# Kernel tuning notes

Measured on AMD Instinct MI355X. Metric: run time of the kernel, lower is better.

Reference implementation:

```python
import jax, jax.numpy as jnp
import numpy as np

B, R, T = 32, 256, 4096  # shots, receivers, time samples; P = T prob grid
EPS = 1e-8


def _trapz(y, t):
    # trapezoidal integral along last axis
    dt = t[1:] - t[:-1]
    return jnp.sum(0.5 * (y[..., 1:] + y[..., :-1]) * dt, axis=-1)


def _cum_trap(y, t):
    # cumulative trapezoid along last axis, prepend 0 -> same length as y
    dt = t[1:] - t[:-1]
    incr = 0.5 * (y[..., 1:] + y[..., :-1]) * dt
    c = jnp.cumsum(incr, axis=-1)
    return jnp.concatenate([jnp.zeros_like(c[..., :1]), c], axis=-1)


def _renorm(x, t):
    # square + trapz-normalize each trace to a probability density over t
    pdf = x * x + EPS
    return pdf / _trapz(pdf, t)[..., None]


def setup_inputs() -> dict:
    key = jax.random.key(0)
    k1, k2 = jax.random.split(key)
    traces = 0.5 * jax.random.normal(k1, (B, R, T), dtype=jnp.float32)
    t = jnp.arange(T, dtype=jnp.float32) * 1e-3
    p = jnp.linspace(0.0, 1.0, T, dtype=jnp.float32)  # probability grid
    # q_raw = true_quantile(obs_data, t, p): invert the observed CDF per trace
    obs = 0.5 * jax.random.normal(k2, (B, R, T), dtype=jnp.float32)
    obs_pdf = _renorm(obs, t)
    obs_cdf = _cum_trap(obs_pdf, t)  # strictly increasing (pdf > 0)
    q_raw = jax.vmap(lambda c: jnp.interp(p, c, t))(obs_cdf.reshape(-1, T))
    q_raw = q_raw.reshape(B, R, T).astype(jnp.float32)
    return {"traces": traces, "t": t, "p": p, "q_raw": q_raw}


def reference(traces, t, p, q_raw):
    pdf = _renorm(traces, t)          # [B,R,T]
    cdf = _cum_trap(pdf, t)           # [B,R,T], in [0,1]
    # quantile lookup: interpolate each trace's quantile table at its cdf values
    cdf_f = cdf.reshape(-1, T)
    q_f = q_raw.reshape(-1, T)
    transport = jax.vmap(jnp.interp, in_axes=(0, None, 0))(cdf_f, p, q_f)
    transport = transport.reshape(pdf.shape)
    diff = t - transport
    loss = jnp.sum(_trapz(diff * diff * pdf, t))
    return loss
```

## Files before the change

### kernel.cpp

```cpp
#include <hip/hip_runtime.h>

#define TT 4096
#define BLK 256
#define PER 16
#define TPB 8
#define EPSV 1e-8f

__device__ __forceinline__ void async_q16(const float* __restrict__ g, float* l) {
  __builtin_amdgcn_global_load_lds(
      (const __attribute__((address_space(1))) void*)g,
      (__attribute__((address_space(3))) void*)l,
      16, 0, 0);
}

__global__ __launch_bounds__(BLK, 4) void w2_loss_kernel(
    const float* __restrict__ traces,
    const float* __restrict__ q_raw,
    float* __restrict__ part) {
  __shared__ float qb[2][TT];
  __shared__ float wave_sums[4];
  __shared__ float wave_red[4];

  const int tid = threadIdx.x;
  const int wv = tid >> 6;
  const int lane = tid & 63;
  const long trace0 = (long)blockIdx.x * TPB;
  const int base = tid * PER;

  {
    const float* qr = q_raw + trace0 * (long)TT;
#pragma unroll
    for (int j = 0; j < 4; ++j) {
      const int c = (wv * 4 + j) * 256;
      async_q16(qr + c + lane * 4, &qb[0][c]);
    }
  }
  float4 trv[4];
  float nb;
  {
    const float* tr = traces + trace0 * (long)TT;
    const float4* tr4 = (const float4*)(tr + base);
#pragma unroll
    for (int j = 0; j < 4; ++j) trv[j] = tr4[j];
    nb = (base + PER < TT) ? tr[base + PER] : 0.0f;
  }

  for (int k = 0; k < TPB; ++k) {
    const int buf = k & 1;
    const long trace = trace0 + k;

    float s[PER + 1];
#pragma unroll
    for (int j = 0; j < 4; ++j) {
      s[4 * j + 0] = trv[j].x * trv[j].x + EPSV;
      s[4 * j + 1] = trv[j].y * trv[j].y + EPSV;
      s[4 * j + 2] = trv[j].z * trv[j].z + EPSV;
      s[4 * j + 3] = trv[j].w * trv[j].w + EPSV;
    }
    s[PER] = (base + PER < TT) ? (nb * nb + EPSV) : 0.0f;

    float lc[PER + 1];
    lc[0] = 0.0f;
#pragma unroll
    for (int m = 0; m < PER; ++m) {
      float t0 = (float)(base + m) * 1e-3f;
      float t1 = (float)(base + m + 1) * 1e-3f;
      float incr = (base + m < TT - 1) ? 0.5f * (s[m] + s[m + 1]) * (t1 - t0)
                                       : 0.0f;
      lc[m + 1] = lc[m] + incr;
    }
    const float tot = lc[PER];

    float v = tot;
#pragma unroll
    for (int off = 1; off < 64; off <<= 1) {
      float n = __shfl_up(v, off, 64);
      if (lane >= off) v += n;
    }
    if (lane == 63) wave_sums[wv] = v;
    __syncthreads();

    if (k + 1 < TPB) {
      const float* qr_n = q_raw + (trace + 1) * (long)TT;
#pragma unroll
      for (int j = 0; j < 4; ++j) {
        const int c = (wv * 4 + j) * 256;
        async_q16(qr_n + c + lane * 4, &qb[buf ^ 1][c]);
      }
      const float* tr_n = traces + (trace + 1) * (long)TT;
      const float4* tr4_n = (const float4*)(tr_n + base);
#pragma unroll
      for (int j = 0; j < 4; ++j) trv[j] = tr4_n[j];
      nb = (base + PER < TT) ? tr_n[base + PER] : 0.0f;
    }

    float wave_off = 0.0f;
    if (wv > 0) wave_off += wave_sums[0];
    if (wv > 1) wave_off += wave_sums[1];
    if (wv > 2) wave_off += wave_sums[2];
    const float excl = (v - tot) + wave_off;
    const float norm = wave_sums[0] + wave_sums[1] + wave_sums[2] + wave_sums[3];
    const float inv_norm = 1.0f / norm;

    const float* __restrict__ lq = qb[buf];
    float local = 0.0f;
#pragma unroll
    for (int m = 0; m < PER; ++m) {
      float x = (excl + lc[m]) * inv_norm;
      float u = x * (float)(TT - 1);
      int i0 = (int)floorf(u);
      i0 = (i0 < 0) ? 0 : ((i0 > TT - 2) ? TT - 2 : i0);
      float f = u - (float)i0;
      f = fminf(fmaxf(f, 0.0f), 1.0f);
      float q0 = lq[i0];
      float q1 = lq[i0 + 1];
      float transport = q0 + f * (q1 - q0);
      float tm = (float)(base + m) * 1e-3f;
      float d = tm - transport;
      float tlo = (float)((base + m == 0) ? 0 : (base + m - 1)) * 1e-3f;
      float thi = (float)((base + m == TT - 1) ? (TT - 1) : (base + m + 1)) * 1e-3f;
      float w = 0.5f * (thi - tlo);
      local += d * d * s[m] * w;
    }
    local *= inv_norm;

#pragma unroll
    for (int off = 32; off > 0; off >>= 1) local += __shfl_down(local, off, 64);
    if (lane == 0) wave_red[wv] = local;
    __syncthreads();
    if (tid == 0) {
      part[trace] = wave_red[0] + wave_red[1] + wave_red[2] + wave_red[3];
    }
  }
}

__global__ __launch_bounds__(BLK) void reduce_kernel(
    const float* __restrict__ part, float* __restrict__ out, int n) {
  __shared__ float wave_red[4];
  const int tid = threadIdx.x;
  float local = 0.0f;
  for (int i = tid; i < n; i += BLK) local += part[i];
#pragma unroll
  for (int off = 32; off > 0; off >>= 1) local += __shfl_down(local, off, 64);
  if ((tid & 63) == 0) wave_red[tid >> 6] = local;
  __syncthreads();
  if (tid == 0) out[0] = wave_red[0] + wave_red[1] + wave_red[2] + wave_red[3];
}

extern "C" void kernel_launch(void* const* d_in, const int* in_sizes, int n_in,
                              void* d_out, int out_size, void* d_ws, size_t ws_size,
                              hipStream_t stream) {
  const float* traces = (const float*)d_in[0];
  const float* q_raw  = (const float*)d_in[3];
  float* out = (float*)d_out;
  float* part = (float*)d_ws;

  const int n_traces = in_sizes[0] / TT;
  const int n_blocks = n_traces / TPB;
  w2_loss_kernel<<<n_blocks, BLK, 0, stream>>>(traces, q_raw, part);
  reduce_kernel<<<1, BLK, 0, stream>>>(part, out, n_traces);
}
```

Measured before the change: 295.7 us.

## Cut LDS and registers to raise occupancy, single-buffer quantile table

Halves traces per block and drops the double-buffered quantile table to one LDS buffer. The launch bound now asks for twice as many resident blocks. The per-element partial CDF array is no longer stored; it is recomputed on the fly in the interpolation loop, and the squared values are kept in place in the float4 registers. Trace loads stay double-buffered, but the next quantile table is only fetched after the block's final barrier. The aim is latency hiding through occupancy instead of in-block overlap, at the cost of less prefetch overlap for the q table and some redundant arithmetic.

```diff
diff --git a/kernel.cpp b/kernel.cpp
--- a/kernel.cpp
+++ b/kernel.cpp
@@ -3,21 +3,29 @@
 #define TT 4096
 #define BLK 256
 #define PER 16
-#define TPB 8
+#define TPB 4
 #define EPSV 1e-8f
 
-__device__ __forceinline__ void async_q16(const float* __restrict__ g, float* l) {
+__device__ __forceinline__ void async_q16(const float* g, float* l) {
   __builtin_amdgcn_global_load_lds(
       (const __attribute__((address_space(1))) void*)g,
-      (__attribute__((address_space(3))) void*)l,
-      16, 0, 0);
+      (__attribute__((address_space(3))) void*)l, 16, 0, 0);
 }
 
-__global__ __launch_bounds__(BLK, 4) void w2_loss_kernel(
+__device__ __forceinline__ float fcomp(const float4& v, int c) {
+  switch (c) {
+    case 0: return v.x;
+    case 1: return v.y;
+    case 2: return v.z;
+    default: return v.w;
+  }
+}
+
+__global__ __launch_bounds__(BLK, 8) void w2_loss_kernel(
     const float* __restrict__ traces,
     const float* __restrict__ q_raw,
     float* __restrict__ part) {
-  __shared__ float qb[2][TT];
+  __shared__ float qb[TT];
   __shared__ float wave_sums[4];
   __shared__ float wave_red[4];
 
@@ -27,49 +35,50 @@
   const long trace0 = (long)blockIdx.x * TPB;
   const int base = tid * PER;
 
+  float4 trv[2][4];
+  float nbuf[2];
   {
+    const float* tr = traces + trace0 * (long)TT;
+    const float4* tr4 = (const float4*)(tr + base);
+#pragma unroll
+    for (int j = 0; j < 4; ++j) trv[0][j] = tr4[j];
+    nbuf[0] = (tid < BLK - 1) ? tr[base + PER] : 0.0f;
     const float* qr = q_raw + trace0 * (long)TT;
 #pragma unroll
     for (int j = 0; j < 4; ++j) {
       const int c = (wv * 4 + j) * 256;
-      async_q16(qr + c + lane * 4, &qb[0][c]);
+      async_q16(qr + c + lane * 4, &qb[c]);
     }
   }
-  float4 trv[4];
-  float nb;
-  {
-    const float* tr = traces + trace0 * (long)TT;
-    const float4* tr4 = (const float4*)(tr + base);
+
 #pragma unroll
-    for (int j = 0; j < 4; ++j) trv[j] = tr4[j];
-    nb = (base + PER < TT) ? tr[base + PER] : 0.0f;
-  }
-
   for (int k = 0; k < TPB; ++k) {
-    const int buf = k & 1;
+    const int cur = k & 1, nxt = cur ^ 1;
     const long trace = trace0 + k;
 
-    float s[PER + 1];
 #pragma unroll
     for (int j = 0; j < 4; ++j) {
-      s[4 * j + 0] = trv[j].x * trv[j].x + EPSV;
-      s[4 * j + 1] = trv[j].y * trv[j].y + EPSV;
-      s[4 * j + 2] = trv[j].z * trv[j].z + EPSV;
-      s[4 * j + 3] = trv[j].w * trv[j].w + EPSV;
+      trv[cur][j].x = trv[cur][j].x * trv[cur][j].x + EPSV;
+      trv[cur][j].y = trv[cur][j].y * trv[cur][j].y + EPSV;
+      trv[cur][j].z = trv[cur][j].z * trv[cur][j].z + EPSV;
+      trv[cur][j].w = trv[cur][j].w * trv[cur][j].w + EPSV;
     }
-    s[PER] = (base + PER < TT) ? (nb * nb + EPSV) : 0.0f;
+    const float s16 = (tid < BLK - 1) ? (nbuf[cur] * nbuf[cur] + EPSV) : 0.0f;
 
-    float lc[PER + 1];
-    lc[0] = 0.0f;
+    float tot = 0.0f;
+    {
+      float t0 = (float)base * 1e-3f;
 #pragma unroll
-    for (int m = 0; m < PER; ++m) {
-      float t0 = (float)(base + m) * 1e-3f;
-      float t1 = (float)(base + m + 1) * 1e-3f;
-      float incr = (base + m < TT - 1) ? 0.5f * (s[m] + s[m + 1]) * (t1 - t0)
-                                       : 0.0f;
-      lc[m + 1] = lc[m] + incr;
+      for (int m = 0; m < PER; ++m) {
+        float t1 = (float)(base + m + 1) * 1e-3f;
+        float sm = fcomp(trv[cur][m >> 2], m & 3);
+        float sm1 = (m < PER - 1) ? fcomp(trv[cur][(m + 1) >> 2], (m + 1) & 3) : s16;
+        float incr = 0.5f * (sm + sm1) * (t1 - t0);
+        if (m == PER - 1) incr = (tid < BLK - 1) ? incr : 0.0f;
+        tot = tot + incr;
+        t0 = t1;
+      }
     }
-    const float tot = lc[PER];
 
     float v = tot;
 #pragma unroll
@@ -80,20 +89,6 @@
     if (lane == 63) wave_sums[wv] = v;
     __syncthreads();
 
-    if (k + 1 < TPB) {
-      const float* qr_n = q_raw + (trace + 1) * (long)TT;
-#pragma unroll
-      for (int j = 0; j < 4; ++j) {
-        const int c = (wv * 4 + j) * 256;
-        async_q16(qr_n + c + lane * 4, &qb[buf ^ 1][c]);
-      }
-      const float* tr_n = traces + (trace + 1) * (long)TT;
-      const float4* tr4_n = (const float4*)(tr_n + base);
-#pragma unroll
-      for (int j = 0; j < 4; ++j) trv[j] = tr4_n[j];
-      nb = (base + PER < TT) ? tr_n[base + PER] : 0.0f;
-    }
-
     float wave_off = 0.0f;
     if (wv > 0) wave_off += wave_sums[0];
     if (wv > 1) wave_off += wave_sums[1];
@@ -102,25 +97,44 @@
     const float norm = wave_sums[0] + wave_sums[1] + wave_sums[2] + wave_sums[3];
     const float inv_norm = 1.0f / norm;
 
-    const float* __restrict__ lq = qb[buf];
+    if (k + 1 < TPB) {
+      const float* trn = traces + (trace + 1) * (long)TT;
+      const float4* tr4n = (const float4*)(trn + base);
+#pragma unroll
+      for (int j = 0; j < 4; ++j) trv[nxt][j] = tr4n[j];
+      nbuf[nxt] = (tid < BLK - 1) ? trn[base + PER] : 0.0f;
+    }
+
     float local = 0.0f;
+    {
+      float tlo = (tid == 0) ? 0.0f : (float)(base - 1) * 1e-3f;
+      float tm = (float)base * 1e-3f;
+      float lcm = 0.0f;
 #pragma unroll
-    for (int m = 0; m < PER; ++m) {
-      float x = (excl + lc[m]) * inv_norm;
-      float u = x * (float)(TT - 1);
-      int i0 = (int)floorf(u);
-      i0 = (i0 < 0) ? 0 : ((i0 > TT - 2) ? TT - 2 : i0);
-      float f = u - (float)i0;
-      f = fminf(fmaxf(f, 0.0f), 1.0f);
-      float q0 = lq[i0];
-      float q1 = lq[i0 + 1];
-      float transport = q0 + f * (q1 - q0);
-      float tm = (float)(base + m) * 1e-3f;
-      float d = tm - transport;
-      float tlo = (float)((base + m == 0) ? 0 : (base + m - 1)) * 1e-3f;
-      float thi = (float)((base + m == TT - 1) ? (TT - 1) : (base + m + 1)) * 1e-3f;
-      float w = 0.5f * (thi - tlo);
-      local += d * d * s[m] * w;
+      for (int m = 0; m < PER; ++m) {
+        float thi = (float)(base + m + 1) * 1e-3f;
+        float thi_w = thi;
+        if (m == PER - 1) thi_w = (tid == BLK - 1) ? tm : thi;
+        float x = (excl + lcm) * inv_norm;
+        float u = x * (float)(TT - 1);
+        int i0 = (int)u;
+        i0 = (i0 > TT - 2) ? TT - 2 : i0;
+        float f = u - (float)i0;
+        f = fminf(f, 1.0f);
+        float q0 = qb[i0];
+        float q1 = qb[i0 + 1];
+        float transport = q0 + f * (q1 - q0);
+        float d = tm - transport;
+        float w = 0.5f * (thi_w - tlo);
+        local += d * d * fcomp(trv[cur][m >> 2], m & 3) * w;
+        if (m < PER - 1) {
+          float sm = fcomp(trv[cur][m >> 2], m & 3);
+          float sm1 = fcomp(trv[cur][(m + 1) >> 2], (m + 1) & 3);
+          lcm = lcm + 0.5f * (sm + sm1) * (thi - tm);
+        }
+        tlo = tm;
+        tm = thi;
+      }
     }
     local *= inv_norm;
 
@@ -130,6 +144,14 @@
     __syncthreads();
     if (tid == 0) {
       part[trace] = wave_red[0] + wave_red[1] + wave_red[2] + wave_red[3];
+    }
+    if (k + 1 < TPB) {
+      const float* qrn = q_raw + (trace + 1) * (long)TT;
+#pragma unroll
+      for (int j = 0; j < 4; ++j) {
+        const int c = (wv * 4 + j) * 256;
+        async_q16(qrn + c + lane * 4, &qb[c]);
+      }
     }
   }
 }
```

Measured after the change: 358.0 us. 21.1% more time.
